# Kernel optimization log

Hardware: AMD Instinct MI355X
Metric: run time of the kernel (lower is better)

The kernel has to match this reference:

```python
import jax, jax.numpy as jnp
import numpy as np

B, S, H = 16, 2048, 768
D_VOCAB, C_VOCAB, U_VOCAB = 512, 512, 50000
D_DIM, C_DIM, MIX_CD = 128, 128, 128


def setup_inputs() -> dict:
    key = jax.random.key(0)
    ks = jax.random.split(key, 11)
    initrange = 0.1
    return {
        "seqs": jax.random.normal(ks[0], (B, S, H), dtype=jnp.float32),
        "d": jax.random.randint(ks[1], (B, S - 1), 0, D_VOCAB),
        "c": jax.random.randint(ks[2], (B, S - 1), 0, C_VOCAB),
        "u": jax.random.randint(ks[3], (B, S), 0, U_VOCAB),
        # embedding tables (torch init: uniform(-0.1, 0.1))
        "E_d": jax.random.uniform(ks[4], (D_VOCAB, D_DIM), jnp.float32, -initrange, initrange),
        "E_c": jax.random.uniform(ks[5], (C_VOCAB, C_DIM), jnp.float32, -initrange, initrange),
        "E_u": jax.random.uniform(ks[6], (U_VOCAB, H), jnp.float32, -initrange, initrange),
        # Linear weights, torch layout [out, in], no bias
        "W_cd": jax.random.normal(ks[7], (MIX_CD, D_DIM + C_DIM), dtype=jnp.float32) * 0.02,
        "W_hid": jax.random.normal(ks[8], (H, 2 * H), dtype=jnp.float32) * 0.02,
        "W_cdh": jax.random.normal(ks[9], (H, MIX_CD + H), dtype=jnp.float32) * 0.02,
    }


def reference(seqs, d, c, u, E_d, E_c, E_u, W_cd, W_hid, W_cdh):
    de = E_d[d]                      # [B, S-1, d_dim]
    ce = E_c[c]                      # [B, S-1, c_dim]
    ue = E_u[u]                      # [B, S, H]
    seqs_u = seqs + ue               # [B, S, H]
    # relu(Linear(cat(d, c)))
    d_c = jax.nn.relu(jnp.einsum('bsi,oi->bso', jnp.concatenate([de, ce], axis=-1), W_cd))
    # adjacent pairs: stack([seqs_u[:, i:i+2]]) then flatten last two dims == cat of shifted views
    pairs = jnp.concatenate([seqs_u[:, :-1], seqs_u[:, 1:]], axis=-1)  # [B, S-1, 2H]
    ph = jax.nn.relu(jnp.einsum('bsi,oi->bso', pairs, W_hid))          # [B, S-1, H]
    m = jax.nn.relu(jnp.einsum('bsi,oi->bso', jnp.concatenate([ph, d_c], axis=-1), W_cdh))  # [B, S-1, H]
    # loop: seqs_u[:, i] += (m[:, i] if i < S-1) + (m[:, i-1] if i > 1)
    # -> two shifted vectorized adds (note: i > 1, so m[:, 0] is NOT added at i=1)
    out = seqs_u.at[:, :-1].add(m)
    out = out.at[:, 2:].add(m[:, 1:])
    return out
```

## Files before the change

### kernel.cpp

```cpp
#include <hip/hip_runtime.h>
#include <hip/hip_bf16.h>
#include <cstdint>
#include <cstddef>

#define B_SZ   16
#define S_LEN  2048
#define H_DIM  768
#define M_ROWS (B_SZ * (S_LEN - 1))

typedef __attribute__((ext_vector_type(8))) __bf16 bf16x8;
typedef __attribute__((ext_vector_type(8))) unsigned short ushort8;
typedef __attribute__((ext_vector_type(4))) float floatx4;

__device__ __forceinline__ float bf2f(unsigned short h) {
  union { unsigned u; float f; } v; v.u = ((unsigned)h) << 16; return v.f;
}
__device__ __forceinline__ unsigned short f2bf(float f) {
  union { float f; unsigned u; } v; v.f = f;
  unsigned u = v.u + 0x7fffu + ((v.u >> 16) & 1u);
  return (unsigned short)(u >> 16);
}

__device__ __forceinline__ void load_lds16(const void* g, void* l) {
  __builtin_amdgcn_global_load_lds(
      (const __attribute__((address_space(1))) void*)g,
      (__attribute__((address_space(3))) void*)l, 16, 0, 0);
}

#define N_ED   (512 * 128)
#define N_EC   (512 * 128)
#define N_WCD  (128 * 256)
#define N_WHID (768 * 1536)
#define N_WCDH (768 * 896)
#define N_CONV (N_ED + N_EC + N_WCD + N_WHID + N_WCDH)

__global__ void convert_weights_kernel(const float* __restrict__ Ed,
                                       const float* __restrict__ Ec,
                                       const float* __restrict__ Wcd,
                                       const float* __restrict__ Whid,
                                       const float* __restrict__ Wcdh,
                                       unsigned short* __restrict__ ed_b,
                                       unsigned short* __restrict__ ec_b,
                                       unsigned short* __restrict__ wcd_b,
                                       unsigned short* __restrict__ whid_b,
                                       unsigned short* __restrict__ wcdh_b) {
  long i = ((long)blockIdx.x * blockDim.x + threadIdx.x) * 8;
  const float* s; unsigned short* dst; long off;
  if (i < N_ED)                            { s = Ed;   dst = ed_b;   off = i; }
  else if (i < N_ED + N_EC)                { s = Ec;   dst = ec_b;   off = i - N_ED; }
  else if (i < N_ED + N_EC + N_WCD)        { s = Wcd;  dst = wcd_b;  off = i - (N_ED + N_EC); }
  else if (i < N_ED + N_EC + N_WCD + N_WHID) { s = Whid; dst = whid_b; off = i - (N_ED + N_EC + N_WCD); }
  else                                     { s = Wcdh; dst = wcdh_b; off = i - (N_ED + N_EC + N_WCD + N_WHID); }
  floatx4 v0 = *(const floatx4*)(s + off);
  floatx4 v1 = *(const floatx4*)(s + off + 4);
  ushort8 o;
#pragma unroll
  for (int t = 0; t < 4; ++t) { o[t] = f2bf(v0[t]); o[t + 4] = f2bf(v1[t]); }
  *(ushort8*)(dst + off) = o;
}

__global__ void embed_add_kernel(const float* __restrict__ seqs,
                                 const int* __restrict__ u,
                                 const float* __restrict__ Eu,
                                 float* __restrict__ out,
                                 unsigned short* __restrict__ sub, int nchunks) {
  int c = blockIdx.x * blockDim.x + threadIdx.x;
  if (c >= nchunks) return;
  int row = c / 96;
  int hc  = c - row * 96;
  int uid = u[row];
  const floatx4* sp = (const floatx4*)seqs + (size_t)c * 2;
  const floatx4* ep = (const floatx4*)(Eu + (size_t)uid * H_DIM + hc * 8);
  floatx4 a0 = sp[0], a1 = sp[1];
  floatx4 b0 = ep[0], b1 = ep[1];
  floatx4 r0, r1; ushort8 ob;
#pragma unroll
  for (int t = 0; t < 4; ++t) {
    r0[t] = a0[t] + b0[t];
    r1[t] = a1[t] + b1[t];
    ob[t] = f2bf(r0[t]); ob[t + 4] = f2bf(r1[t]);
  }
  floatx4* op = (floatx4*)out + (size_t)c * 2;
  op[0] = r0; op[1] = r1;
  *((ushort8*)sub + c) = ob;
}

template <int MODE, int K, int LDW, int NOUT>
__global__ __launch_bounds__(256)
void gemm_nt_relu(const unsigned short* __restrict__ A0,
                  const unsigned short* __restrict__ A1,
                  const int* __restrict__ idx0,
                  const int* __restrict__ idx1,
                  const unsigned short* __restrict__ W,
                  unsigned short* __restrict__ out) {
  constexpr int NT = NOUT / 128;

  const int nwg = gridDim.x;
  const int q = nwg >> 3, r = nwg & 7;
  const int xcd = blockIdx.x & 7, lid = blockIdx.x >> 3;
  const int wgid = (xcd < r ? xcd * (q + 1) : r * (q + 1) + (xcd - r) * q) + lid;
  const int bm = wgid / NT;
  const int bn = wgid - bm * NT;

  __shared__ unsigned short As[128 * 64];
  __shared__ unsigned short Ws[128 * 64];

  const int tid  = threadIdx.x;
  const int lane = tid & 63;
  const int wave = tid >> 6;
  const int lrow = lane >> 3;
  const int cc   = lane & 7;
  const int scc  = cc ^ lrow;
  const int wm   = wave >> 1, wn = wave & 1;
  const int m16  = lane & 15, quad = lane >> 4;
  const int rxor = m16 & 7;

  floatx4 acc[4][4] = {};

  for (int kt = 0; kt < K / 64; ++kt) {
    const int colbase = kt * 64;
#pragma unroll
    for (int it = 0; it < 4; ++it) {
      int row = it * 32 + wave * 8 + lrow;
      int n = bm * 128 + row;
      if (n >= M_ROWS) n = M_ROWS - 1;
      const unsigned short* g;
      if constexpr (MODE == 0) {
        if (colbase < 128) g = A0 + (size_t)idx0[n] * 128 + colbase + scc * 8;
        else               g = A1 + (size_t)idx1[n] * 128 + (colbase - 128) + scc * 8;
      } else if constexpr (MODE == 1) {
        int b = n / (S_LEN - 1);
        int s = n - b * (S_LEN - 1);
        int grow = b * S_LEN + s + (colbase >= H_DIM ? 1 : 0);
        int gcol = (colbase >= H_DIM ? colbase - H_DIM : colbase) + scc * 8;
        g = A0 + (size_t)grow * H_DIM + gcol;
      } else {
        if (colbase < H_DIM) g = A0 + (size_t)n * H_DIM + colbase + scc * 8;
        else                 g = A1 + (size_t)n * 128 + (colbase - H_DIM) + scc * 8;
      }
      load_lds16(g, &As[(it * 256 + wave * 64) * 8]);

      int wrow = bn * 128 + row;
      const unsigned short* gw = W + (size_t)wrow * LDW + colbase + scc * 8;
      load_lds16(gw, &Ws[(it * 256 + wave * 64) * 8]);
    }
    __syncthreads();

#pragma unroll
    for (int kk = 0; kk < 64; kk += 32) {
      const int k8 = kk >> 3;
      bf16x8 a[4], b[4];
#pragma unroll
      for (int i = 0; i < 4; ++i) {
        int rr = wm * 64 + i * 16 + m16;
        a[i] = *(const bf16x8*)&As[rr * 64 + (((k8 + quad) ^ rxor) << 3)];
      }
#pragma unroll
      for (int j = 0; j < 4; ++j) {
        int rr = wn * 64 + j * 16 + m16;
        b[j] = *(const bf16x8*)&Ws[rr * 64 + (((k8 + quad) ^ rxor) << 3)];
      }
#pragma unroll
      for (int i = 0; i < 4; ++i)
#pragma unroll
        for (int j = 0; j < 4; ++j)
          acc[i][j] = __builtin_amdgcn_mfma_f32_16x16x32_bf16(a[i], b[j], acc[i][j], 0, 0, 0);
    }
    __syncthreads();
  }

#pragma unroll
  for (int i = 0; i < 4; ++i) {
#pragma unroll
    for (int r2 = 0; r2 < 4; ++r2) {
      int row = bm * 128 + wm * 64 + i * 16 + quad * 4 + r2;
      if (row < M_ROWS) {
#pragma unroll
        for (int j = 0; j < 4; ++j) {
          int col = bn * 128 + wn * 64 + j * 16 + m16;
          out[(size_t)row * NOUT + col] = f2bf(fmaxf(acc[i][j][r2], 0.0f));
        }
      }
    }
  }
}

__global__ void final_add_kernel(const unsigned short* __restrict__ mm,
                                 float* __restrict__ out, int nchunks) {
  int c = blockIdx.x * blockDim.x + threadIdx.x;
  if (c >= nchunks) return;
  int row = c / 96;
  int hc  = c - row * 96;
  int b = row >> 11;
  int s = row & (S_LEN - 1);
  floatx4* op = (floatx4*)out + (size_t)c * 2;
  floatx4 v0 = op[0], v1 = op[1];
  int mrow = b * (S_LEN - 1) + s;
  if (s < S_LEN - 1) {
    ushort8 x = *(const ushort8*)(mm + (size_t)mrow * H_DIM + hc * 8);
#pragma unroll
    for (int t = 0; t < 4; ++t) { v0[t] += bf2f(x[t]); v1[t] += bf2f(x[t + 4]); }
  }
  if (s >= 2) {
    ushort8 x = *(const ushort8*)(mm + (size_t)(mrow - 1) * H_DIM + hc * 8);
#pragma unroll
    for (int t = 0; t < 4; ++t) { v0[t] += bf2f(x[t]); v1[t] += bf2f(x[t + 4]); }
  }
  op[0] = v0; op[1] = v1;
}

extern "C" void kernel_launch(void* const* d_in, const int* in_sizes, int n_in,
                              void* d_out, int out_size, void* d_ws, size_t ws_size,
                              hipStream_t stream) {
  const float* seqs  = (const float*)d_in[0];
  const int*   d_idx = (const int*)d_in[1];
  const int*   c_idx = (const int*)d_in[2];
  const int*   u_idx = (const int*)d_in[3];
  const float* E_d   = (const float*)d_in[4];
  const float* E_c   = (const float*)d_in[5];
  const float* E_u   = (const float*)d_in[6];
  const float* W_cd  = (const float*)d_in[7];
  const float* W_hid = (const float*)d_in[8];
  const float* W_cdh = (const float*)d_in[9];
  float* out = (float*)d_out;

  unsigned short* sub   = (unsigned short*)d_ws;
  unsigned short* ph    = sub   + (size_t)B_SZ * S_LEN * H_DIM;
  unsigned short* mmb   = ph    + (size_t)M_ROWS * H_DIM;
  unsigned short* dc    = mmb   + (size_t)M_ROWS * H_DIM;
  unsigned short* ed_b  = dc    + (size_t)M_ROWS * 128;
  unsigned short* ec_b  = ed_b  + N_ED;
  unsigned short* wcd_b = ec_b  + N_EC;
  unsigned short* whid_b = wcd_b + N_WCD;
  unsigned short* wcdh_b = whid_b + N_WHID;

  const int nchunks = B_SZ * S_LEN * (H_DIM / 8);
  const int mtiles = (M_ROWS + 127) / 128;

  convert_weights_kernel<<<N_CONV / (256 * 8), 256, 0, stream>>>(
      E_d, E_c, W_cd, W_hid, W_cdh, ed_b, ec_b, wcd_b, whid_b, wcdh_b);
  embed_add_kernel<<<(nchunks + 255) / 256, 256, 0, stream>>>(seqs, u_idx, E_u, out, sub, nchunks);
  gemm_nt_relu<0, 256, 256, 128><<<mtiles * 1, 256, 0, stream>>>(ed_b, ec_b, d_idx, c_idx, wcd_b, dc);
  gemm_nt_relu<1, 1536, 1536, 768><<<mtiles * 6, 256, 0, stream>>>(sub, nullptr, nullptr, nullptr, whid_b, ph);
  gemm_nt_relu<2, 896, 896, 768><<<mtiles * 6, 256, 0, stream>>>(ph, dc, nullptr, nullptr, wcdh_b, mmb);
  final_add_kernel<<<(nchunks + 255) / 256, 256, 0, stream>>>(mmb, out, nchunks);
}
```

Measured before the change: 552.5 us.

## Double-buffer LDS tiles in GEMM and precompute per-row global pointers

Adds a second LDS buffer for the A and W tiles so the next K-tile's global-to-LDS loads are issued while MFMAs run on the current tile, with one barrier per iteration. Per-row source pointers, including the embedding gather indices and the batch/sequence split, are now computed once before the K loop instead of on every tile. It also raises wave priority around the MFMA block with s_setprio. The cost is double the LDS per workgroup (64KB), which may reduce occupancy.

```diff
diff --git a/kernel.cpp b/kernel.cpp
--- a/kernel.cpp
+++ b/kernel.cpp
@@ -94,6 +94,7 @@
                   const unsigned short* __restrict__ W,
                   unsigned short* __restrict__ out) {
   constexpr int NT = NOUT / 128;
+  constexpr int NTILES = K / 64;
 
   const int nwg = gridDim.x;
   const int q = nwg >> 3, r = nwg & 7;
@@ -102,8 +103,8 @@
   const int bm = wgid / NT;
   const int bn = wgid - bm * NT;
 
-  __shared__ unsigned short As[128 * 64];
-  __shared__ unsigned short Ws[128 * 64];
+  __shared__ unsigned short As[2][128 * 64];
+  __shared__ unsigned short Ws[2][128 * 64];
 
   const int tid  = threadIdx.x;
   const int lane = tid & 63;
@@ -115,56 +116,78 @@
   const int m16  = lane & 15, quad = lane >> 4;
   const int rxor = m16 & 7;
 
+  const unsigned short* gA[4];
+  const unsigned short* gA2[4];
+  const unsigned short* gW[4];
+#pragma unroll
+  for (int it = 0; it < 4; ++it) {
+    int row = it * 32 + wave * 8 + lrow;
+    int n = bm * 128 + row;
+    if (n >= M_ROWS) n = M_ROWS - 1;
+    if constexpr (MODE == 0) {
+      gA[it]  = A0 + (size_t)idx0[n] * 128 + scc * 8;
+      gA2[it] = A1 + (size_t)idx1[n] * 128 + scc * 8;
+    } else if constexpr (MODE == 1) {
+      int b = n / (S_LEN - 1);
+      int s = n - b * (S_LEN - 1);
+      gA[it]  = A0 + (size_t)(b * S_LEN + s) * H_DIM + scc * 8;
+      gA2[it] = gA[it];
+    } else {
+      gA[it]  = A0 + (size_t)n * H_DIM + scc * 8;
+      gA2[it] = A1 + (size_t)n * 128 + scc * 8;
+    }
+    int wrow = bn * 128 + row;
+    gW[it] = W + (size_t)wrow * LDW + scc * 8;
+  }
+
   floatx4 acc[4][4] = {};
 
-  for (int kt = 0; kt < K / 64; ++kt) {
+  auto STAGE = [&](int kt, int buf) {
     const int colbase = kt * 64;
 #pragma unroll
     for (int it = 0; it < 4; ++it) {
-      int row = it * 32 + wave * 8 + lrow;
-      int n = bm * 128 + row;
-      if (n >= M_ROWS) n = M_ROWS - 1;
       const unsigned short* g;
       if constexpr (MODE == 0) {
-        if (colbase < 128) g = A0 + (size_t)idx0[n] * 128 + colbase + scc * 8;
-        else               g = A1 + (size_t)idx1[n] * 128 + (colbase - 128) + scc * 8;
+        g = (colbase < 128) ? gA[it] + colbase : gA2[it] + (colbase - 128);
       } else if constexpr (MODE == 1) {
-        int b = n / (S_LEN - 1);
-        int s = n - b * (S_LEN - 1);
-        int grow = b * S_LEN + s + (colbase >= H_DIM ? 1 : 0);
-        int gcol = (colbase >= H_DIM ? colbase - H_DIM : colbase) + scc * 8;
-        g = A0 + (size_t)grow * H_DIM + gcol;
+        g = gA[it] + colbase;
       } else {
-        if (colbase < H_DIM) g = A0 + (size_t)n * H_DIM + colbase + scc * 8;
-        else                 g = A1 + (size_t)n * 128 + (colbase - H_DIM) + scc * 8;
-      }
-      load_lds16(g, &As[(it * 256 + wave * 64) * 8]);
-
-      int wrow = bn * 128 + row;
-      const unsigned short* gw = W + (size_t)wrow * LDW + colbase + scc * 8;
-      load_lds16(gw, &Ws[(it * 256 + wave * 64) * 8]);
-    }
-    __syncthreads();
-
-#pragma unroll
-    for (int kk = 0; kk < 64; kk += 32) {
-      const int k8 = kk >> 3;
+        g = (colbase < H_DIM) ? gA[it] + colbase : gA2[it] + (colbase - H_DIM);
+      }
+      load_lds16(g, &As[buf][(it * 256 + wave * 64) * 8]);
+      load_lds16(gW[it] + colbase, &Ws[buf][(it * 256 + wave * 64) * 8]);
+    }
+  };
+
+  STAGE(0, 0);
+  __syncthreads();
+
+  for (int kt = 0; kt < NTILES; ++kt) {
+    const int cur = kt & 1;
+    if (kt + 1 < NTILES) STAGE(kt + 1, cur ^ 1);
+
+    const unsigned short* as = As[cur];
+    const unsigned short* ws = Ws[cur];
+#pragma unroll
+    for (int k8 = 0; k8 < 8; k8 += 4) {
       bf16x8 a[4], b[4];
 #pragma unroll
       for (int i = 0; i < 4; ++i) {
         int rr = wm * 64 + i * 16 + m16;
-        a[i] = *(const bf16x8*)&As[rr * 64 + (((k8 + quad) ^ rxor) << 3)];
+        a[i] = *(const bf16x8*)&as[rr * 64 + (((k8 + quad) ^ rxor) << 3)];
       }
 #pragma unroll
       for (int j = 0; j < 4; ++j) {
         int rr = wn * 64 + j * 16 + m16;
-        b[j] = *(const bf16x8*)&Ws[rr * 64 + (((k8 + quad) ^ rxor) << 3)];
-      }
+        b[j] = *(const bf16x8*)&ws[rr * 64 + (((k8 + quad) ^ rxor) << 3)];
+      }
+      __builtin_amdgcn_s_setprio(1);
 #pragma unroll
       for (int i = 0; i < 4; ++i)
 #pragma unroll
         for (int j = 0; j < 4; ++j)
           acc[i][j] = __builtin_amdgcn_mfma_f32_16x16x32_bf16(a[i], b[j], acc[i][j], 0, 0, 0);
+      __builtin_amdgcn_s_setprio(0);
     }
     __syncthreads();
   }
```

New measurement: 549.3 us. No clear change (-0.6%).
